# Kernel optimization log

Hardware: AMD Instinct MI355X
Metric: run time of the kernel (lower is better)

The kernel has to match this reference:

```python
import jax, jax.numpy as jnp
import numpy as np

N_NODES = 50000
N_EDGES = 200000
N_GRAPH = 1024
H = 128          # hidden_channels
POS = 48         # pos_offset
NF = 256         # num_filters in SchNetInteraction
L = 5            # n_layers
NFF = 512
MAX_ITEM = 300


def ssp(v):
    # shifted softplus used by SchNet
    return jax.nn.softplus(v) - jnp.log(2.0)


def setup_inputs() -> dict:
    key = jax.random.key(0)
    ks = iter(jax.random.split(key, 40))
    s = 0.05
    inp = {}
    inp['x'] = jax.random.randint(next(ks), (N_NODES,), 0, MAX_ITEM)
    inp['edge_index'] = jax.random.randint(next(ks), (2, N_EDGES), 0, N_NODES)
    inp['edge_attr'] = jax.random.normal(next(ks), (N_EDGES, 4), jnp.float32)
    inp['batch'] = jnp.sort(jax.random.randint(next(ks), (N_NODES,), 0, N_GRAPH))
    inp['pos'] = jax.random.normal(next(ks), (N_NODES, 3), jnp.float32)
    # embedding / projection params
    vert = jax.random.normal(next(ks), (MAX_ITEM + 1, H - POS), jnp.float32) * s
    inp['vert_emb'] = vert.at[MAX_ITEM].set(0.0)  # padding_idx
    inp['pos_w'] = jax.random.normal(next(ks), (POS, 3), jnp.float32) * s
    inp['edge_w'] = jax.random.normal(next(ks), (H, 4), jnp.float32) * s
    # per-layer SchNetInteraction params (stacked over L)
    inp['filt_w1'] = jax.random.normal(next(ks), (L, NF, H), jnp.float32) * s
    inp['filt_b1'] = jnp.zeros((L, NF), jnp.float32)
    inp['filt_w2'] = jax.random.normal(next(ks), (L, NF, NF), jnp.float32) * s
    inp['filt_b2'] = jnp.zeros((L, NF), jnp.float32)
    inp['lin1_w'] = jax.random.normal(next(ks), (L, NF, H), jnp.float32) * s
    inp['lin2_w'] = jax.random.normal(next(ks), (L, H, NF), jnp.float32) * s
    inp['lin2_b'] = jnp.zeros((L, H), jnp.float32)
    inp['lin3_w'] = jax.random.normal(next(ks), (L, H, H), jnp.float32) * s
    inp['lin3_b'] = jnp.zeros((L, H), jnp.float32)
    # per-layer edge MLP: Linear(edge_ch + in_ch -> in_ch) + Tanh
    inp['em_w'] = jax.random.normal(next(ks), (L, H, 2 * H), jnp.float32) * s
    inp['em_b'] = jnp.zeros((L, H), jnp.float32)
    # head
    inp['head_w1'] = jax.random.normal(next(ks), (NFF, H), jnp.float32) * s
    inp['head_b1'] = jnp.zeros((NFF,), jnp.float32)
    inp['head_w2'] = jax.random.normal(next(ks), (1, NFF), jnp.float32) * s
    inp['head_b2'] = jnp.zeros((1,), jnp.float32)
    return inp


def _forward(x, edge_index, edge_attr, batch, pos, vert_emb, pos_w, edge_w,
             filt_w1, filt_b1, filt_w2, filt_b2, lin1_w, lin2_w, lin2_b,
             lin3_w, lin3_b, em_w, em_b, head_w1, head_b1, head_w2, head_b2):
    n = x.shape[0]
    src, dst = edge_index[0], edge_index[1]
    h = jnp.concatenate([vert_emb[x], pos @ pos_w.T], axis=-1)  # [N, H]
    ea = edge_attr @ edge_w.T                                    # [E, H]
    for i in range(L):
        # SchNetInteraction / CFConv: per-edge filter MLP, gather, scatter-sum
        W = ssp(ea @ filt_w1[i].T + filt_b1[i]) @ filt_w2[i].T + filt_b2[i]  # [E, NF]
        hj = (h @ lin1_w[i].T)[src]                                          # [E, NF]
        agg = jax.ops.segment_sum(hj * W, dst, num_segments=n)               # [N, NF]
        out = ssp(agg @ lin2_w[i].T + lin2_b[i]) @ lin3_w[i].T + lin3_b[i]   # [N, H]
        h = jax.nn.relu(out) + h  # relu + residual skip
        # edge MLP update (always active in ResGraphModule)
        ea = jnp.tanh(jnp.concatenate([ea, h[src] + h[dst]], axis=-1) @ em_w[i].T + em_b[i]) + ea
    # global mean pool over graphs
    ssum = jax.ops.segment_sum(h, batch, num_segments=N_GRAPH)               # [G, H]
    cnt = jax.ops.segment_sum(jnp.ones((n,), h.dtype), batch, num_segments=N_GRAPH)
    g = ssum / jnp.maximum(cnt, 1.0)[:, None]
    # head: Linear -> GELU (exact, as torch default) -> Dropout(eval) -> Linear
    y = jax.nn.gelu(g @ head_w1.T + head_b1, approximate=False) @ head_w2.T + head_b2
    return y  # [G, 1]


def reference(x, edge_index, edge_attr, batch, pos, vert_emb, pos_w, edge_w,
              filt_w1, filt_b1, filt_w2, filt_b2, lin1_w, lin2_w, lin2_b,
              lin3_w, lin3_b, em_w, em_b, head_w1, head_b1, head_w2, head_b2):
    return _forward(x, edge_index, edge_attr, batch, pos, vert_emb, pos_w, edge_w,
                    filt_w1, filt_b1, filt_w2, filt_b2, lin1_w, lin2_w, lin2_b,
                    lin3_w, lin3_b, em_w, em_b, head_w1, head_b1, head_w2, head_b2)
```

## Files before the change

### kernel.cpp

```cpp
#include <hip/hip_runtime.h>
#include <hip/hip_bf16.h>
#include <math.h>

#define N_NODES 50000
#define N_EDGES 200000
#define N_GRAPH 1024
#define HC      128
#define NFC     256
#define NLAYER  5
#define NFFC    512

typedef short bf16x8 __attribute__((ext_vector_type(8)));
typedef float f4v    __attribute__((ext_vector_type(4)));

__device__ __forceinline__ float ssp_f(float x) {
  float e = __expf(-fabsf(x));
  return fmaxf(x, 0.0f) + __logf(1.0f + e) - 0.69314718055994530942f;
}
__device__ __forceinline__ float tanh_f(float x) {
  float e = __expf(2.0f * fabsf(x));
  float t = 1.0f - 2.0f * __builtin_amdgcn_rcpf(e + 1.0f);
  return copysignf(t, x);
}
__device__ __forceinline__ unsigned short f2bf(float x) {
  union { float f; unsigned u; } v; v.f = x;
  unsigned r = v.u + 0x7fff + ((v.u >> 16) & 1);
  return (unsigned short)(r >> 16);
}
__device__ __forceinline__ float bf2f(unsigned short b) {
  union { unsigned u; float f; } v; v.u = (unsigned)b << 16; return v.f;
}

__device__ __forceinline__ int swzA(int row, int col) {
  return (row << 7) + (((col >> 3) ^ (row & 7)) << 3) + (col & 7);
}
__device__ __forceinline__ int swzT(int row, int col) {
  return (row << 8) + (((col >> 3) ^ (row & 7)) << 3) + (col & 7);
}

__global__ void zero_kernel(float4* __restrict__ p, int n4) {
  int i = blockIdx.x * blockDim.x + threadIdx.x;
  if (i < n4) p[i] = make_float4(0.f, 0.f, 0.f, 0.f);
}
__global__ void zeroi_kernel(int* __restrict__ p, int n) {
  int i = blockIdx.x * blockDim.x + threadIdx.x;
  if (i < n) p[i] = 0;
}

__global__ void hist_kernel(const int* __restrict__ ei, int* __restrict__ deg) {
  int e = blockIdx.x * blockDim.x + threadIdx.x;
  if (e < N_EDGES) atomicAdd(&deg[ei[N_EDGES + e]], 1);
}
__global__ void scan1_kernel(const int* __restrict__ deg, int* __restrict__ excl,
                             int* __restrict__ bsum, int n) {
  __shared__ int buf[256];
  const int tid = threadIdx.x;
  const int i = blockIdx.x * 256 + tid;
  int v = (i < n) ? deg[i] : 0;
  buf[tid] = v;
  __syncthreads();
  for (int s = 1; s < 256; s <<= 1) {
    int t = (tid >= s) ? buf[tid - s] : 0;
    __syncthreads();
    buf[tid] += t;
    __syncthreads();
  }
  if (i < n) excl[i] = buf[tid] - v;
  if (tid == 255) bsum[blockIdx.x] = buf[255];
}
__global__ void scan2_kernel(int* __restrict__ bsum, int nb) {
  __shared__ int buf[256];
  const int tid = threadIdx.x;
  int v = (tid < nb) ? bsum[tid] : 0;
  buf[tid] = v;
  __syncthreads();
  for (int s = 1; s < 256; s <<= 1) {
    int t = (tid >= s) ? buf[tid - s] : 0;
    __syncthreads();
    buf[tid] += t;
    __syncthreads();
  }
  if (tid < nb) bsum[tid] = buf[tid] - v;
}
__global__ void scan3_kernel(int* __restrict__ excl, const int* __restrict__ bsum, int n) {
  int i = blockIdx.x * 256 + threadIdx.x;
  if (i < n) excl[i] += bsum[blockIdx.x];
}
__global__ void perm_kernel(const int* __restrict__ ei, int* __restrict__ cursor,
                            int* __restrict__ perm) {
  int e = blockIdx.x * blockDim.x + threadIdx.x;
  if (e < N_EDGES) {
    int d = ei[N_EDGES + e];
    int p = atomicAdd(&cursor[d], 1);
    perm[p] = e;
  }
}
__global__ void eperm_kernel(const int* __restrict__ ei, const int* __restrict__ perm,
                             int* __restrict__ eiPs, int* __restrict__ eiPd,
                             int* __restrict__ ipos) {
  int p = blockIdx.x * blockDim.x + threadIdx.x;
  if (p < N_EDGES) {
    int e = perm[p];
    eiPs[p] = ei[e];
    eiPd[p] = ei[N_EDGES + e];
    ipos[e] = p;
  }
}

__global__ void wconv_kernel(const float* __restrict__ w,
                             unsigned short* __restrict__ hi, int n) {
  int i = blockIdx.x * blockDim.x + threadIdx.x;
  if (i < n) hi[i] = f2bf(w[i]);
}

__global__ void embed_kernel(const int* __restrict__ x, const float* __restrict__ pos,
                             const float* __restrict__ vert, const float* __restrict__ posw,
                             unsigned short* __restrict__ h) {
  int n = blockIdx.x;
  int c = threadIdx.x;
  float v;
  if (c < 80) {
    v = vert[(size_t)x[n] * 80 + c];
  } else {
    int j = c - 80;
    v = pos[n*3+0]*posw[j*3+0] + pos[n*3+1]*posw[j*3+1] + pos[n*3+2]*posw[j*3+2];
  }
  h[(size_t)n*HC + c] = f2bf(v);
}

__global__ void edgeproj_kernel(const float* __restrict__ eattr, const float* __restrict__ ew,
                                unsigned short* __restrict__ eaP,
                                const int* __restrict__ ipos) {
  int idx = blockIdx.x * blockDim.x + threadIdx.x;
  if (idx >= N_EDGES * HC) return;
  int e = idx >> 7, c = idx & 127;
  const float* a = eattr + (size_t)e*4;
  const float* w = ew + (size_t)c*4;
  eaP[(size_t)ipos[e]*HC + c] = f2bf(a[0]*w[0] + a[1]*w[1] + a[2]*w[2] + a[3]*w[3]);
}

__global__ __launch_bounds__(256, 4) void emlite_kernel(
    unsigned short* eaP,
    const unsigned short* __restrict__ Bh,
    const float* __restrict__ bias,
    const int* __restrict__ eiPs, const int* __restrict__ eiPd,
    const unsigned short* __restrict__ hfeat)
{
  __shared__ unsigned short ldsA[64 * 128];
  __shared__ unsigned short ldsH[64 * 128];

  const int tid  = threadIdx.x;
  const int m0   = blockIdx.x * 64;
  const int lane = tid & 63, wave = tid >> 6;
  const int quad = lane >> 4, l16 = lane & 15;
  const int r = tid >> 2, cb = (tid & 3) * 32;

  const int e = m0 + r;
  const int s = eiPs[e], d = eiPd[e];

  {
    const unsigned short* ap = eaP + (size_t)e * HC + cb;
#pragma unroll
    for (int q = 0; q < 4; q++)
      *(bf16x8*)&ldsA[swzA(r, cb + q*8)] = *(const bf16x8*)(ap + q*8);
    const unsigned short* p1 = hfeat + (size_t)s * HC + cb;
    const unsigned short* p2 = hfeat + (size_t)d * HC + cb;
    unsigned short x1[32], x2[32], th[32];
#pragma unroll
    for (int q = 0; q < 4; q++) {
      *(bf16x8*)&x1[q*8] = *(const bf16x8*)(p1 + q*8);
      *(bf16x8*)&x2[q*8] = *(const bf16x8*)(p2 + q*8);
    }
#pragma unroll
    for (int j = 0; j < 32; j++) th[j] = f2bf(bf2f(x1[j]) + bf2f(x2[j]));
#pragma unroll
    for (int q = 0; q < 4; q++)
      *(bf16x8*)&ldsH[swzA(r, cb + q*8)] = *(bf16x8*)&th[q*8];
  }

  const f4v zf = {0.f, 0.f, 0.f, 0.f};
  f4v acc[4][2];
#pragma unroll
  for (int mt = 0; mt < 4; mt++) { acc[mt][0] = zf; acc[mt][1] = zf; }

  __syncthreads();

#pragma unroll
  for (int nt = 0; nt < 2; nt++) {
    const size_t brow = (size_t)(wave*32 + nt*16 + l16);
#pragma unroll
    for (int kk = 0; kk < 128; kk += 32) {
      bf16x8 b = *(const bf16x8*)&Bh[brow * 2*HC + kk + quad*8];
#pragma unroll
      for (int mt = 0; mt < 4; mt++) {
        bf16x8 a = *(const bf16x8*)&ldsA[swzA(mt*16 + l16, kk + quad*8)];
        acc[mt][nt] = __builtin_amdgcn_mfma_f32_16x16x32_bf16(a, b, acc[mt][nt], 0, 0, 0);
      }
    }
#pragma unroll
    for (int kk = 0; kk < 128; kk += 32) {
      bf16x8 b = *(const bf16x8*)&Bh[brow * 2*HC + HC + kk + quad*8];
#pragma unroll
      for (int mt = 0; mt < 4; mt++) {
        bf16x8 a = *(const bf16x8*)&ldsH[swzA(mt*16 + l16, kk + quad*8)];
        acc[mt][nt] = __builtin_amdgcn_mfma_f32_16x16x32_bf16(a, b, acc[mt][nt], 0, 0, 0);
      }
    }
  }

#pragma unroll
  for (int nt = 0; nt < 2; nt++) {
    const int col = wave*32 + nt*16 + l16;
    const float bz = bias[col];
#pragma unroll
    for (int mt = 0; mt < 4; mt++) {
      const int rowb = mt*16 + quad*4;
#pragma unroll
      for (int rr = 0; rr < 4; rr++) {
        const size_t idx = (size_t)(m0 + rowb + rr) * HC + col;
        eaP[idx] = f2bf(tanh_f(acc[mt][nt][rr] + bz) + bf2f(ldsA[swzA(rowb + rr, col)]));
      }
    }
  }
}

__global__ __launch_bounds__(256, 2) void nodeup_kernel(
    float* __restrict__ agg,
    const unsigned short* __restrict__ L2h,
    const float* __restrict__ b2,
    const unsigned short* __restrict__ L3h,
    const float* __restrict__ b3,
    unsigned short* h)
{
  __shared__ unsigned short ldsS[128 * 256];

  const int tid  = threadIdx.x;
  const int m0   = blockIdx.x * 128;
  const int lane = tid & 63, wave = tid >> 6;
  const int quad = lane >> 4, l16 = lane & 15;
  const int wm = (wave >> 1) * 64, wn = (wave & 1) * 64;
  const int r  = tid >> 1;
  const int ch = (tid & 1) * 128;

  const bool mok = (m0 + r) < N_NODES;

  if (mok) {
    const float* ap = agg + (size_t)(m0 + r) * NFC + ch;
#pragma unroll
    for (int g = 0; g < 16; g++) {
      float4 v0 = *(const float4*)(ap + g*8);
      float4 v1 = *(const float4*)(ap + g*8 + 4);
      unsigned short th[8];
      th[0] = f2bf(v0.x); th[1] = f2bf(v0.y); th[2] = f2bf(v0.z); th[3] = f2bf(v0.w);
      th[4] = f2bf(v1.x); th[5] = f2bf(v1.y); th[6] = f2bf(v1.z); th[7] = f2bf(v1.w);
      *(bf16x8*)&ldsS[swzT(r, ch + g*8)] = *(bf16x8*)th;
    }
    float4* zp = (float4*)(agg + (size_t)(m0 + r) * NFC + ch);
    const float4 z4 = make_float4(0.f, 0.f, 0.f, 0.f);
#pragma unroll
    for (int g = 0; g < 32; g++) zp[g] = z4;
  } else {
    const bf16x8 zb = {0, 0, 0, 0, 0, 0, 0, 0};
#pragma unroll
    for (int g = 0; g < 16; g++) *(bf16x8*)&ldsS[swzT(r, ch + g*8)] = zb;
  }

  const f4v zf = {0.f, 0.f, 0.f, 0.f};
  f4v acc[4][4];
#pragma unroll
  for (int i = 0; i < 4; i++)
#pragma unroll
    for (int j = 0; j < 4; j++) acc[i][j] = zf;

  __syncthreads();

  for (int kk = 0; kk < NFC; kk += 32) {
    bf16x8 b[4];
#pragma unroll
    for (int nt = 0; nt < 4; nt++) {
      const size_t brow = (size_t)(wn + nt*16 + l16);
      b[nt] = *(const bf16x8*)&L2h[brow * NFC + kk + quad*8];
    }
    bf16x8 a[4];
#pragma unroll
    for (int t = 0; t < 4; t++)
      a[t] = *(const bf16x8*)&ldsS[swzT(wm + t*16 + l16, kk + quad*8)];
#pragma unroll
    for (int mt = 0; mt < 4; mt++)
#pragma unroll
      for (int nt = 0; nt < 4; nt++)
        acc[mt][nt] = __builtin_amdgcn_mfma_f32_16x16x32_bf16(a[mt], b[nt], acc[mt][nt], 0, 0, 0);
  }
  __syncthreads();

#pragma unroll
  for (int nt = 0; nt < 4; nt++) {
    const int col = wn + nt*16 + l16;
    const float bz = b2[col];
#pragma unroll
    for (int mt = 0; mt < 4; mt++) {
      const int rowb = wm + mt*16 + quad*4;
#pragma unroll
      for (int rr = 0; rr < 4; rr++)
        ldsS[swzT(rowb+rr, col)] = f2bf(ssp_f(acc[mt][nt][rr] + bz));
    }
  }
  __syncthreads();

  f4v acc2[4][4];
#pragma unroll
  for (int i = 0; i < 4; i++)
#pragma unroll
    for (int j = 0; j < 4; j++) acc2[i][j] = zf;

  for (int kk = 0; kk < HC; kk += 32) {
    bf16x8 b[4];
#pragma unroll
    for (int nt = 0; nt < 4; nt++) {
      const size_t brow = (size_t)(wn + nt*16 + l16);
      b[nt] = *(const bf16x8*)&L3h[brow * HC + kk + quad*8];
    }
    bf16x8 a[4];
#pragma unroll
    for (int t = 0; t < 4; t++)
      a[t] = *(const bf16x8*)&ldsS[swzT(wm + t*16 + l16, kk + quad*8)];
#pragma unroll
    for (int mt = 0; mt < 4; mt++)
#pragma unroll
      for (int nt = 0; nt < 4; nt++)
        acc2[mt][nt] = __builtin_amdgcn_mfma_f32_16x16x32_bf16(a[mt], b[nt], acc2[mt][nt], 0, 0, 0);
  }

#pragma unroll
  for (int nt = 0; nt < 4; nt++) {
    const int ncol = wn + nt*16 + l16;
    const float bz = b3[ncol];
#pragma unroll
    for (int mt = 0; mt < 4; mt++) {
      const int mb = wm + mt*16 + quad*4;
#pragma unroll
      for (int rr = 0; rr < 4; rr++) {
        const int m = m0 + mb + rr;
        if (m < N_NODES) {
          const size_t idx = (size_t)m * HC + ncol;
          h[idx] = f2bf(fmaxf(acc2[mt][nt][rr] + bz, 0.f) + bf2f(h[idx]));
        }
      }
    }
  }
}

__device__ __forceinline__ int sigma_row(int r) {
  return ((r >> 2) & 3) * 16 + (r >> 4) * 4 + (r & 3);
}
__global__ __launch_bounds__(256, 3) void ffs_kernel(
    const unsigned short* __restrict__ eaP,
    const unsigned short* __restrict__ l1h,
    const unsigned short* __restrict__ fw1h,
    const float* __restrict__ fb1,
    const unsigned short* __restrict__ fw2h,
    const float* __restrict__ fb2,
    const int* __restrict__ eiPs, const int* __restrict__ eiPd,
    const unsigned short* __restrict__ hfeat, float* __restrict__ agg)
{
  __shared__ unsigned short ldsA[64 * 128];
  __shared__ unsigned short ldsT[64 * 256];
  __shared__ int sD[64];

  const int tid  = threadIdx.x;
  const int m0   = blockIdx.x * 64;
  const int lane = tid & 63, wave = tid >> 6;
  const int quad = lane >> 4, l16 = lane & 15;
  const int r = tid >> 2, cb = (tid & 3) * 32;
  const int sp = m0 + sigma_row(r);

  const int s = eiPs[sp];
  bf16x8 hreg[4];
  {
    const unsigned short* hp = hfeat + (size_t)s * HC + cb;
#pragma unroll
    for (int q = 0; q < 4; q++) hreg[q] = *(const bf16x8*)(hp + q*8);
  }
  if (tid < 64) sD[tid] = eiPd[m0 + sigma_row(tid)];

  {
    const unsigned short* ap = eaP + (size_t)sp * HC + cb;
#pragma unroll
    for (int q = 0; q < 4; q++)
      *(bf16x8*)&ldsA[swzA(r, cb + q*8)] = *(const bf16x8*)(ap + q*8);
  }

  const f4v zf = {0.f, 0.f, 0.f, 0.f};
  __syncthreads();

  for (int p = 0; p < 4; p++) {
    f4v tacc[4];
#pragma unroll
    for (int mt = 0; mt < 4; mt++) tacc[mt] = zf;
    const size_t b1row = (size_t)(p*64 + wave*16 + l16);
#pragma unroll
    for (int kk = 0; kk < 128; kk += 32) {
      bf16x8 b = *(const bf16x8*)&fw1h[b1row * HC + kk + quad*8];
#pragma unroll
      for (int mt = 0; mt < 4; mt++) {
        bf16x8 a = *(const bf16x8*)&ldsA[swzA(mt*16 + l16, kk + quad*8)];
        tacc[mt] = __builtin_amdgcn_mfma_f32_16x16x32_bf16(a, b, tacc[mt], 0, 0, 0);
      }
    }
    const int col = p*64 + wave*16 + l16;
    const float bz = fb1[col];
#pragma unroll
    for (int mt = 0; mt < 4; mt++) {
      const int rowb = mt*16 + quad*4;
#pragma unroll
      for (int rr = 0; rr < 4; rr++)
        ldsT[swzT(rowb+rr, col)] = f2bf(ssp_f(tacc[mt][rr] + bz));
    }
  }
  __syncthreads();

#pragma unroll
  for (int q = 0; q < 4; q++)
    *(bf16x8*)&ldsA[swzA(r, cb + q*8)] = hreg[q];

  f4v wacc[4][4];
#pragma unroll
  for (int mt = 0; mt < 4; mt++)
#pragma unroll
    for (int nt = 0; nt < 4; nt++) wacc[mt][nt] = zf;

  __builtin_amdgcn_s_setprio(1);
  for (int p = 0; p < 4; p++) {
#pragma unroll
    for (int kc = 0; kc < 2; kc++) {
      bf16x8 a_[4];
#pragma unroll
      for (int mt = 0; mt < 4; mt++)
        a_[mt] = *(const bf16x8*)&ldsT[swzT(mt*16 + l16, p*64 + kc*32 + quad*8)];
#pragma unroll
      for (int nt = 0; nt < 4; nt++) {
        const size_t brow = (size_t)(wave*64 + nt*16 + l16);
        bf16x8 b = *(const bf16x8*)&fw2h[brow * NFC + p*64 + kc*32 + quad*8];
#pragma unroll
        for (int mt = 0; mt < 4; mt++)
          wacc[mt][nt] = __builtin_amdgcn_mfma_f32_16x16x32_bf16(a_[mt], b, wacc[mt][nt], 0, 0, 0);
      }
    }
  }
  __builtin_amdgcn_s_setprio(0);
  __syncthreads();

  f4v hacc[4][4];
#pragma unroll
  for (int mt = 0; mt < 4; mt++)
#pragma unroll
    for (int nt = 0; nt < 4; nt++) hacc[mt][nt] = zf;

#pragma unroll
  for (int kk = 0; kk < 128; kk += 32) {
    bf16x8 a_[4];
#pragma unroll
    for (int mt = 0; mt < 4; mt++)
      a_[mt] = *(const bf16x8*)&ldsA[swzA(mt*16 + l16, kk + quad*8)];
#pragma unroll
    for (int nt = 0; nt < 4; nt++) {
      const size_t brow = (size_t)(wave*64 + nt*16 + l16);
      bf16x8 b = *(const bf16x8*)&l1h[brow * HC + kk + quad*8];
#pragma unroll
      for (int mt = 0; mt < 4; mt++)
        hacc[mt][nt] = __builtin_amdgcn_mfma_f32_16x16x32_bf16(a_[mt], b, hacc[mt][nt], 0, 0, 0);
    }
  }

#pragma unroll
  for (int nt = 0; nt < 4; nt++) {
    const int col = wave*64 + nt*16 + l16;
    const float bz = fb2[col];
    float accum = 0.f;
    int prev = -1;
    bool firstrun = true;
#pragma unroll
    for (int mt = 0; mt < 4; mt++) {
#pragma unroll
      for (int rr = 0; rr < 4; rr++) {
        const int prow = mt*16 + quad*4 + rr;
        const int d = sD[prow];
        const float v = (wacc[mt][nt][rr] + bz) * hacc[mt][nt][rr];
        if (d != prev) {
          if (prev >= 0) {
            if (firstrun) atomicAdd(&agg[(size_t)prev * NFC + col], accum);
            else          agg[(size_t)prev * NFC + col] = accum;
            firstrun = false;
          }
          accum = v; prev = d;
        } else {
          accum += v;
        }
      }
    }
    atomicAdd(&agg[(size_t)prev * NFC + col], accum);
  }
}

__global__ __launch_bounds__(256) void poolhead_kernel(
    const int* __restrict__ batch, const unsigned short* __restrict__ h,
    const float* __restrict__ w1, const float* __restrict__ b1,
    const float* __restrict__ w2, const float* __restrict__ b2,
    float* __restrict__ y)
{
  __shared__ float gs[HC];
  __shared__ float red[256];
  const int g = blockIdx.x;
  const int tid = threadIdx.x;

  int lo = 0, hi = N_NODES;
  while (lo < hi) { int m = (lo + hi) >> 1; if (batch[m] < g) lo = m + 1; else hi = m; }
  int lo2 = lo, hi2 = N_NODES;
  while (lo2 < hi2) { int m = (lo2 + hi2) >> 1; if (batch[m] < g + 1) lo2 = m + 1; else hi2 = m; }
  const int cnt = lo2 - lo;

  if (tid < HC) {
    float s = 0.f;
    for (int i = lo; i < lo2; i++) s += bf2f(h[(size_t)i * HC + tid]);
    gs[tid] = s / (float)max(cnt, 1);
  }
  __syncthreads();

  float partial = 0.f;
  for (int f = tid; f < NFFC; f += 256) {
    float acc = b1[f];
    const float* wr = w1 + (size_t)f * HC;
#pragma unroll 8
    for (int k = 0; k < HC; k++) acc = fmaf(gs[k], wr[k], acc);
    float t = 0.5f * acc * (1.0f + erff(acc * 0.70710678118654752440f));
    partial = fmaf(t, w2[f], partial);
  }
  red[tid] = partial;
  __syncthreads();
  for (int s = 128; s > 0; s >>= 1) {
    if (tid < s) red[tid] += red[tid + s];
    __syncthreads();
  }
  if (tid == 0) y[g] = red[0] + b2[0];
}

extern "C" void kernel_launch(void* const* d_in, const int* in_sizes, int n_in,
                              void* d_out, int out_size, void* d_ws, size_t ws_size,
                              hipStream_t stream) {
  const int*   x     = (const int*)  d_in[0];
  const int*   ei    = (const int*)  d_in[1];
  const float* eattr = (const float*)d_in[2];
  const int*   batch = (const int*)  d_in[3];
  const float* pos   = (const float*)d_in[4];
  const float* vert  = (const float*)d_in[5];
  const float* posw  = (const float*)d_in[6];
  const float* edgew = (const float*)d_in[7];
  const float* fw1   = (const float*)d_in[8];
  const float* fb1   = (const float*)d_in[9];
  const float* fw2   = (const float*)d_in[10];
  const float* fb2   = (const float*)d_in[11];
  const float* l1w   = (const float*)d_in[12];
  const float* l2w   = (const float*)d_in[13];
  const float* l2b   = (const float*)d_in[14];
  const float* l3w   = (const float*)d_in[15];
  const float* l3b   = (const float*)d_in[16];
  const float* emw   = (const float*)d_in[17];
  const float* emb   = (const float*)d_in[18];
  const float* hw1   = (const float*)d_in[19];
  const float* hb1   = (const float*)d_in[20];
  const float* hw2   = (const float*)d_in[21];
  const float* hb2   = (const float*)d_in[22];
  float* out = (float*)d_out;

  char* ws = (char*)d_ws;
  size_t off = 0;
  auto alloc = [&](size_t bytes) { char* p = ws + off; off += (bytes + 511) & ~(size_t)511; return p; };
  unsigned short* eaP = (unsigned short*)alloc((size_t)N_EDGES*HC*2);
  unsigned short* h   = (unsigned short*)alloc((size_t)N_NODES*HC*2);
  float* agg  = (float*)alloc((size_t)N_NODES*NFC*4);
  int* deg    = (int*)alloc((size_t)(N_NODES+1)*4);
  int* cursor = (int*)alloc((size_t)(N_NODES+1)*4);
  int* bsum   = (int*)alloc((size_t)256*4);
  int* perm   = (int*)alloc((size_t)N_EDGES*4);
  int* eiPs   = (int*)alloc((size_t)N_EDGES*4);
  int* eiPd   = (int*)alloc((size_t)N_EDGES*4);
  int* ipos   = (int*)alloc((size_t)N_EDGES*4);
  const int n_fw1 = NLAYER*NFC*HC, n_fw2 = NLAYER*NFC*NFC, n_l1 = NLAYER*NFC*HC;
  const int n_l2 = NLAYER*HC*NFC, n_l3 = NLAYER*HC*HC, n_em = NLAYER*HC*2*HC;
  unsigned short* fw1h = (unsigned short*)alloc((size_t)n_fw1*2);
  unsigned short* fw2h = (unsigned short*)alloc((size_t)n_fw2*2);
  unsigned short* l1h  = (unsigned short*)alloc((size_t)n_l1*2);
  unsigned short* l2h  = (unsigned short*)alloc((size_t)n_l2*2);
  unsigned short* l3h  = (unsigned short*)alloc((size_t)n_l3*2);
  unsigned short* emh  = (unsigned short*)alloc((size_t)n_em*2);

  const int NSCAN = N_NODES + 1;
  const int NB    = (NSCAN + 255) / 256;

  zeroi_kernel<<<(NSCAN+255)/256, 256, 0, stream>>>(deg, NSCAN);
  hist_kernel<<<(N_EDGES+255)/256, 256, 0, stream>>>(ei, deg);
  scan1_kernel<<<NB, 256, 0, stream>>>(deg, cursor, bsum, NSCAN);
  scan2_kernel<<<1, 256, 0, stream>>>(bsum, NB);
  scan3_kernel<<<NB, 256, 0, stream>>>(cursor, bsum, NSCAN);
  perm_kernel<<<(N_EDGES+255)/256, 256, 0, stream>>>(ei, cursor, perm);
  eperm_kernel<<<(N_EDGES+255)/256, 256, 0, stream>>>(ei, perm, eiPs, eiPd, ipos);

  wconv_kernel<<<(n_fw1+255)/256, 256, 0, stream>>>(fw1, fw1h, n_fw1);
  wconv_kernel<<<(n_fw2+255)/256, 256, 0, stream>>>(fw2, fw2h, n_fw2);
  wconv_kernel<<<(n_l1 +255)/256, 256, 0, stream>>>(l1w, l1h, n_l1);
  wconv_kernel<<<(n_l2 +255)/256, 256, 0, stream>>>(l2w, l2h, n_l2);
  wconv_kernel<<<(n_l3 +255)/256, 256, 0, stream>>>(l3w, l3h, n_l3);
  wconv_kernel<<<(n_em +255)/256, 256, 0, stream>>>(emw, emh, n_em);

  const int GN   = (N_NODES + 127) / 128;
  const int GE64 = N_EDGES / 64;

  embed_kernel<<<N_NODES, 128, 0, stream>>>(x, pos, vert, posw, h);
  edgeproj_kernel<<<(N_EDGES*HC + 255)/256, 256, 0, stream>>>(eattr, edgew, eaP, ipos);
  zero_kernel<<<((N_NODES*NFC/4) + 255)/256, 256, 0, stream>>>(
      (float4*)agg, N_NODES*NFC/4);

  for (int i = 0; i < NLAYER; ++i) {
    ffs_kernel<<<GE64, 256, 0, stream>>>(
        eaP, l1h + (size_t)i*NFC*HC,
        fw1h + (size_t)i*NFC*HC, fb1 + (size_t)i*NFC,
        fw2h + (size_t)i*NFC*NFC, fb2 + (size_t)i*NFC,
        eiPs, eiPd, h, agg);
    nodeup_kernel<<<GN, 256, 0, stream>>>(
        agg, l2h + (size_t)i*HC*NFC, l2b + (size_t)i*HC,
        l3h + (size_t)i*HC*HC, l3b + (size_t)i*HC, h);
    if (i < NLAYER - 1) {
      emlite_kernel<<<GE64, 256, 0, stream>>>(
          eaP, emh + (size_t)i*HC*2*HC, emb + (size_t)i*HC,
          eiPs, eiPd, h);
    }
  }

  poolhead_kernel<<<N_GRAPH, 256, 0, stream>>>(batch, h, hw1, hb1, hw2, hb2, out);
}
```

Baseline: 1.485 ms.

## Prefetch weight fragments across MFMA loops and shrink nodeup tile for occupancy

Adds one-step-ahead register prefetch of global B-operand fragments in the edge-MLP, filter (ffs) and node-update kernels, so weight loads overlap MFMA work instead of stalling. The ffs kernel splits its W/H accumulators into two column halves, which cuts live registers. The node-update kernel moves to 64-row tiles with 4 blocks per CU and half the shared memory, doubling the grid. The risk is lower per-block weight reuse and the extra syncs and loop overhead of the half-split.

```diff
diff --git a/kernel.cpp b/kernel.cpp
--- a/kernel.cpp
+++ b/kernel.cpp
@@ -183,28 +183,25 @@
 #pragma unroll
   for (int mt = 0; mt < 4; mt++) { acc[mt][0] = zf; acc[mt][1] = zf; }
 
-  __syncthreads();
-
-#pragma unroll
-  for (int nt = 0; nt < 2; nt++) {
-    const size_t brow = (size_t)(wave*32 + nt*16 + l16);
-#pragma unroll
-    for (int kk = 0; kk < 128; kk += 32) {
-      bf16x8 b = *(const bf16x8*)&Bh[brow * 2*HC + kk + quad*8];
-#pragma unroll
-      for (int mt = 0; mt < 4; mt++) {
-        bf16x8 a = *(const bf16x8*)&ldsA[swzA(mt*16 + l16, kk + quad*8)];
-        acc[mt][nt] = __builtin_amdgcn_mfma_f32_16x16x32_bf16(a, b, acc[mt][nt], 0, 0, 0);
-      }
-    }
-#pragma unroll
-    for (int kk = 0; kk < 128; kk += 32) {
-      bf16x8 b = *(const bf16x8*)&Bh[brow * 2*HC + HC + kk + quad*8];
-#pragma unroll
-      for (int mt = 0; mt < 4; mt++) {
-        bf16x8 a = *(const bf16x8*)&ldsH[swzA(mt*16 + l16, kk + quad*8)];
-        acc[mt][nt] = __builtin_amdgcn_mfma_f32_16x16x32_bf16(a, b, acc[mt][nt], 0, 0, 0);
-      }
+  bf16x8 bn = *(const bf16x8*)&Bh[(size_t)(wave*32 + l16) * 2*HC + quad*8];
+
+  __syncthreads();
+
+#pragma unroll
+  for (int g = 0; g < 16; g++) {
+    const int nt = g >> 3, hf = (g >> 2) & 1, ki = g & 3;
+    bf16x8 bc = bn;
+    if (g < 15) {
+      const int g1 = g + 1;
+      const int nt1 = g1 >> 3, hf1 = (g1 >> 2) & 1, ki1 = g1 & 3;
+      bn = *(const bf16x8*)&Bh[(size_t)(wave*32 + nt1*16 + l16) * 2*HC
+                               + hf1*HC + ki1*32 + quad*8];
+    }
+    const unsigned short* src = hf ? ldsH : ldsA;
+#pragma unroll
+    for (int mt = 0; mt < 4; mt++) {
+      bf16x8 a = *(const bf16x8*)&src[swzA(mt*16 + l16, ki*32 + quad*8)];
+      acc[mt][nt] = __builtin_amdgcn_mfma_f32_16x16x32_bf16(a, bc, acc[mt][nt], 0, 0, 0);
     }
   }
 
@@ -224,7 +221,7 @@
   }
 }
 
-__global__ __launch_bounds__(256, 2) void nodeup_kernel(
+__global__ __launch_bounds__(256, 4) void nodeup_kernel(
     float* __restrict__ agg,
     const unsigned short* __restrict__ L2h,
     const float* __restrict__ b2,
@@ -232,112 +229,121 @@
     const float* __restrict__ b3,
     unsigned short* h)
 {
-  __shared__ unsigned short ldsS[128 * 256];
+  __shared__ unsigned short ldsS[64 * 256];
 
   const int tid  = threadIdx.x;
-  const int m0   = blockIdx.x * 128;
+  const int m0   = blockIdx.x * 64;
   const int lane = tid & 63, wave = tid >> 6;
   const int quad = lane >> 4, l16 = lane & 15;
-  const int wm = (wave >> 1) * 64, wn = (wave & 1) * 64;
-  const int r  = tid >> 1;
-  const int ch = (tid & 1) * 128;
+  const int wn = wave * 32;
+  const int r  = tid >> 2;
+  const int cb2 = (tid & 3) * 64;
 
   const bool mok = (m0 + r) < N_NODES;
 
   if (mok) {
-    const float* ap = agg + (size_t)(m0 + r) * NFC + ch;
-#pragma unroll
-    for (int g = 0; g < 16; g++) {
+    const float* ap = agg + (size_t)(m0 + r) * NFC + cb2;
+#pragma unroll
+    for (int g = 0; g < 8; g++) {
       float4 v0 = *(const float4*)(ap + g*8);
       float4 v1 = *(const float4*)(ap + g*8 + 4);
       unsigned short th[8];
       th[0] = f2bf(v0.x); th[1] = f2bf(v0.y); th[2] = f2bf(v0.z); th[3] = f2bf(v0.w);
       th[4] = f2bf(v1.x); th[5] = f2bf(v1.y); th[6] = f2bf(v1.z); th[7] = f2bf(v1.w);
-      *(bf16x8*)&ldsS[swzT(r, ch + g*8)] = *(bf16x8*)th;
-    }
-    float4* zp = (float4*)(agg + (size_t)(m0 + r) * NFC + ch);
+      *(bf16x8*)&ldsS[swzT(r, cb2 + g*8)] = *(bf16x8*)th;
+    }
+    float4* zp = (float4*)(agg + (size_t)(m0 + r) * NFC + cb2);
     const float4 z4 = make_float4(0.f, 0.f, 0.f, 0.f);
 #pragma unroll
-    for (int g = 0; g < 32; g++) zp[g] = z4;
+    for (int g = 0; g < 16; g++) zp[g] = z4;
   } else {
     const bf16x8 zb = {0, 0, 0, 0, 0, 0, 0, 0};
 #pragma unroll
-    for (int g = 0; g < 16; g++) *(bf16x8*)&ldsS[swzT(r, ch + g*8)] = zb;
+    for (int g = 0; g < 8; g++) *(bf16x8*)&ldsS[swzT(r, cb2 + g*8)] = zb;
   }
 
   const f4v zf = {0.f, 0.f, 0.f, 0.f};
-  f4v acc[4][4];
-#pragma unroll
-  for (int i = 0; i < 4; i++)
-#pragma unroll
-    for (int j = 0; j < 4; j++) acc[i][j] = zf;
-
-  __syncthreads();
-
-  for (int kk = 0; kk < NFC; kk += 32) {
-    bf16x8 b[4];
-#pragma unroll
-    for (int nt = 0; nt < 4; nt++) {
-      const size_t brow = (size_t)(wn + nt*16 + l16);
-      b[nt] = *(const bf16x8*)&L2h[brow * NFC + kk + quad*8];
+  f4v acc[4][2];
+#pragma unroll
+  for (int i = 0; i < 4; i++) { acc[i][0] = zf; acc[i][1] = zf; }
+
+  bf16x8 bn[2];
+#pragma unroll
+  for (int nt = 0; nt < 2; nt++)
+    bn[nt] = *(const bf16x8*)&L2h[(size_t)(wn + nt*16 + l16) * NFC + quad*8];
+
+  __syncthreads();
+
+  for (int kki = 0; kki < 8; kki++) {
+    bf16x8 bc[2] = {bn[0], bn[1]};
+    if (kki < 7) {
+#pragma unroll
+      for (int nt = 0; nt < 2; nt++)
+        bn[nt] = *(const bf16x8*)&L2h[(size_t)(wn + nt*16 + l16) * NFC
+                                      + (kki+1)*32 + quad*8];
     }
     bf16x8 a[4];
 #pragma unroll
     for (int t = 0; t < 4; t++)
-      a[t] = *(const bf16x8*)&ldsS[swzT(wm + t*16 + l16, kk + quad*8)];
+      a[t] = *(const bf16x8*)&ldsS[swzT(t*16 + l16, kki*32 + quad*8)];
 #pragma unroll
     for (int mt = 0; mt < 4; mt++)
 #pragma unroll
-      for (int nt = 0; nt < 4; nt++)
-        acc[mt][nt] = __builtin_amdgcn_mfma_f32_16x16x32_bf16(a[mt], b[nt], acc[mt][nt], 0, 0, 0);
-  }
-  __syncthreads();
-
-#pragma unroll
-  for (int nt = 0; nt < 4; nt++) {
+      for (int nt = 0; nt < 2; nt++)
+        acc[mt][nt] = __builtin_amdgcn_mfma_f32_16x16x32_bf16(a[mt], bc[nt], acc[mt][nt], 0, 0, 0);
+  }
+  __syncthreads();
+
+#pragma unroll
+  for (int nt = 0; nt < 2; nt++) {
     const int col = wn + nt*16 + l16;
     const float bz = b2[col];
 #pragma unroll
     for (int mt = 0; mt < 4; mt++) {
-      const int rowb = wm + mt*16 + quad*4;
+      const int rowb = mt*16 + quad*4;
 #pragma unroll
       for (int rr = 0; rr < 4; rr++)
-        ldsS[swzT(rowb+rr, col)] = f2bf(ssp_f(acc[mt][nt][rr] + bz));
-    }
-  }
-  __syncthreads();
-
-  f4v acc2[4][4];
-#pragma unroll
-  for (int i = 0; i < 4; i++)
-#pragma unroll
-    for (int j = 0; j < 4; j++) acc2[i][j] = zf;
-
-  for (int kk = 0; kk < HC; kk += 32) {
-    bf16x8 b[4];
-#pragma unroll
-    for (int nt = 0; nt < 4; nt++) {
-      const size_t brow = (size_t)(wn + nt*16 + l16);
-      b[nt] = *(const bf16x8*)&L3h[brow * HC + kk + quad*8];
+        ldsS[swzA(rowb+rr, col)] = f2bf(ssp_f(acc[mt][nt][rr] + bz));
+    }
+  }
+
+  bf16x8 b3n[2];
+#pragma unroll
+  for (int nt = 0; nt < 2; nt++)
+    b3n[nt] = *(const bf16x8*)&L3h[(size_t)(wn + nt*16 + l16) * HC + quad*8];
+
+  __syncthreads();
+
+  f4v acc2[4][2];
+#pragma unroll
+  for (int i = 0; i < 4; i++) { acc2[i][0] = zf; acc2[i][1] = zf; }
+
+  for (int kki = 0; kki < 4; kki++) {
+    bf16x8 bc[2] = {b3n[0], b3n[1]};
+    if (kki < 3) {
+#pragma unroll
+      for (int nt = 0; nt < 2; nt++)
+        b3n[nt] = *(const bf16x8*)&L3h[(size_t)(wn + nt*16 + l16) * HC
+                                       + (kki+1)*32 + quad*8];
     }
     bf16x8 a[4];
 #pragma unroll
     for (int t = 0; t < 4; t++)
-      a[t] = *(const bf16x8*)&ldsS[swzT(wm + t*16 + l16, kk + quad*8)];
+      a[t] = *(const bf16x8*)&ldsS[swzA(t*16 + l16, kki*32 + quad*8)];
 #pragma unroll
     for (int mt = 0; mt < 4; mt++)
 #pragma unroll
-      for (int nt = 0; nt < 4; nt++)
-        acc2[mt][nt] = __builtin_amdgcn_mfma_f32_16x16x32_bf16(a[mt], b[nt], acc2[mt][nt], 0, 0, 0);
-  }
-
-#pragma unroll
-  for (int nt = 0; nt < 4; nt++) {
+      for (int nt = 0; nt < 2; nt++)
+        acc2[mt][nt] = __builtin_amdgcn_mfma_f32_16x16x32_bf16(a[mt], bc[nt], acc2[mt][nt], 0, 0, 0);
+  }
+
+#pragma unroll
+  for (int nt = 0; nt < 2; nt++) {
     const int ncol = wn + nt*16 + l16;
     const float bz = b3[ncol];
 #pragma unroll
     for (int mt = 0; mt < 4; mt++) {
-      const int mb = wm + mt*16 + quad*4;
+      const int mb = mt*16 + quad*4;
 #pragma unroll
       for (int rr = 0; rr < 4; rr++) {
         const int m = m0 + mb + rr;
@@ -391,23 +397,31 @@
   }
 
   const f4v zf = {0.f, 0.f, 0.f, 0.f};
+  const int bcol = wave*16 + l16;
+
+  bf16x8 b1n = *(const bf16x8*)&fw1h[(size_t)bcol * HC + quad*8];
+
   __syncthreads();
 
   for (int p = 0; p < 4; p++) {
     f4v tacc[4];
 #pragma unroll
     for (int mt = 0; mt < 4; mt++) tacc[mt] = zf;
-    const size_t b1row = (size_t)(p*64 + wave*16 + l16);
-#pragma unroll
-    for (int kk = 0; kk < 128; kk += 32) {
-      bf16x8 b = *(const bf16x8*)&fw1h[b1row * HC + kk + quad*8];
+#pragma unroll
+    for (int ki = 0; ki < 4; ki++) {
+      bf16x8 bc = b1n;
+      {
+        const int np = (ki < 3) ? p : ((p < 3) ? p + 1 : 3);
+        const int nk = (ki < 3) ? (ki + 1) * 32 : 0;
+        b1n = *(const bf16x8*)&fw1h[(size_t)(np*64 + bcol) * HC + nk + quad*8];
+      }
 #pragma unroll
       for (int mt = 0; mt < 4; mt++) {
-        bf16x8 a = *(const bf16x8*)&ldsA[swzA(mt*16 + l16, kk + quad*8)];
-        tacc[mt] = __builtin_amdgcn_mfma_f32_16x16x32_bf16(a, b, tacc[mt], 0, 0, 0);
+        bf16x8 a = *(const bf16x8*)&ldsA[swzA(mt*16 + l16, ki*32 + quad*8)];
+        tacc[mt] = __builtin_amdgcn_mfma_f32_16x16x32_bf16(a, bc, tacc[mt], 0, 0, 0);
       }
     }
-    const int col = p*64 + wave*16 + l16;
+    const int col = p*64 + bcol;
     const float bz = fb1[col];
 #pragma unroll
     for (int mt = 0; mt < 4; mt++) {
@@ -417,88 +431,113 @@
         ldsT[swzT(rowb+rr, col)] = f2bf(ssp_f(tacc[mt][rr] + bz));
     }
   }
+
+  bf16x8 b2n[2];
+#pragma unroll
+  for (int nt = 0; nt < 2; nt++)
+    b2n[nt] = *(const bf16x8*)&fw2h[(size_t)(wave*64 + nt*16 + l16) * NFC + quad*8];
+  bf16x8 b3n[2];
+#pragma unroll
+  for (int nt = 0; nt < 2; nt++)
+    b3n[nt] = *(const bf16x8*)&l1h[(size_t)(wave*64 + nt*16 + l16) * HC + quad*8];
+
   __syncthreads();
 
 #pragma unroll
   for (int q = 0; q < 4; q++)
     *(bf16x8*)&ldsA[swzA(r, cb + q*8)] = hreg[q];
 
-  f4v wacc[4][4];
-#pragma unroll
-  for (int mt = 0; mt < 4; mt++)
-#pragma unroll
-    for (int nt = 0; nt < 4; nt++) wacc[mt][nt] = zf;
-
-  __builtin_amdgcn_s_setprio(1);
-  for (int p = 0; p < 4; p++) {
-#pragma unroll
-    for (int kc = 0; kc < 2; kc++) {
+  __syncthreads();
+
+  for (int hf = 0; hf < 2; hf++) {
+    f4v wacc[4][2], hacc[4][2];
+#pragma unroll
+    for (int mt = 0; mt < 4; mt++) {
+      wacc[mt][0] = zf; wacc[mt][1] = zf;
+      hacc[mt][0] = zf; hacc[mt][1] = zf;
+    }
+
+    __builtin_amdgcn_s_setprio(1);
+    for (int g = 0; g < 8; g++) {
+      bf16x8 bc[2] = {b2n[0], b2n[1]};
+      if (g < 7) {
+        const int g1 = g + 1;
+        const int off = (g1 >> 1) * 64 + (g1 & 1) * 32;
+#pragma unroll
+        for (int nt = 0; nt < 2; nt++)
+          b2n[nt] = *(const bf16x8*)&fw2h[(size_t)(wave*64 + (hf*2+nt)*16 + l16) * NFC
+                                          + off + quad*8];
+      } else if (hf == 0) {
+#pragma unroll
+        for (int nt = 0; nt < 2; nt++)
+          b2n[nt] = *(const bf16x8*)&fw2h[(size_t)(wave*64 + (2+nt)*16 + l16) * NFC
+                                          + quad*8];
+      }
+      const int off0 = (g >> 1) * 64 + (g & 1) * 32;
       bf16x8 a_[4];
 #pragma unroll
       for (int mt = 0; mt < 4; mt++)
-        a_[mt] = *(const bf16x8*)&ldsT[swzT(mt*16 + l16, p*64 + kc*32 + quad*8)];
-#pragma unroll
-      for (int nt = 0; nt < 4; nt++) {
-        const size_t brow = (size_t)(wave*64 + nt*16 + l16);
-        bf16x8 b = *(const bf16x8*)&fw2h[brow * NFC + p*64 + kc*32 + quad*8];
+        a_[mt] = *(const bf16x8*)&ldsT[swzT(mt*16 + l16, off0 + quad*8)];
+#pragma unroll
+      for (int nt = 0; nt < 2; nt++)
 #pragma unroll
         for (int mt = 0; mt < 4; mt++)
-          wacc[mt][nt] = __builtin_amdgcn_mfma_f32_16x16x32_bf16(a_[mt], b, wacc[mt][nt], 0, 0, 0);
+          wacc[mt][nt] = __builtin_amdgcn_mfma_f32_16x16x32_bf16(a_[mt], bc[nt], wacc[mt][nt], 0, 0, 0);
+    }
+
+    for (int ki = 0; ki < 4; ki++) {
+      bf16x8 bc[2] = {b3n[0], b3n[1]};
+      if (ki < 3) {
+#pragma unroll
+        for (int nt = 0; nt < 2; nt++)
+          b3n[nt] = *(const bf16x8*)&l1h[(size_t)(wave*64 + (hf*2+nt)*16 + l16) * HC
+                                         + (ki+1)*32 + quad*8];
+      } else if (hf == 0) {
+#pragma unroll
+        for (int nt = 0; nt < 2; nt++)
+          b3n[nt] = *(const bf16x8*)&l1h[(size_t)(wave*64 + (2+nt)*16 + l16) * HC
+                                         + quad*8];
       }
-    }
-  }
-  __builtin_amdgcn_s_setprio(0);
-  __syncthreads();
-
-  f4v hacc[4][4];
-#pragma unroll
-  for (int mt = 0; mt < 4; mt++)
-#pragma unroll
-    for (int nt = 0; nt < 4; nt++) hacc[mt][nt] = zf;
-
-#pragma unroll
-  for (int kk = 0; kk < 128; kk += 32) {
-    bf16x8 a_[4];
-#pragma unroll
-    for (int mt = 0; mt < 4; mt++)
-      a_[mt] = *(const bf16x8*)&ldsA[swzA(mt*16 + l16, kk + quad*8)];
-#pragma unroll
-    for (int nt = 0; nt < 4; nt++) {
-      const size_t brow = (size_t)(wave*64 + nt*16 + l16);
-      bf16x8 b = *(const bf16x8*)&l1h[brow * HC + kk + quad*8];
+      bf16x8 a_[4];
 #pragma unroll
       for (int mt = 0; mt < 4; mt++)
-        hacc[mt][nt] = __builtin_amdgcn_mfma_f32_16x16x32_bf16(a_[mt], b, hacc[mt][nt], 0, 0, 0);
-    }
-  }
-
-#pragma unroll
-  for (int nt = 0; nt < 4; nt++) {
-    const int col = wave*64 + nt*16 + l16;
-    const float bz = fb2[col];
-    float accum = 0.f;
-    int prev = -1;
-    bool firstrun = true;
-#pragma unroll
-    for (int mt = 0; mt < 4; mt++) {
-#pragma unroll
-      for (int rr = 0; rr < 4; rr++) {
-        const int prow = mt*16 + quad*4 + rr;
-        const int d = sD[prow];
-        const float v = (wacc[mt][nt][rr] + bz) * hacc[mt][nt][rr];
-        if (d != prev) {
-          if (prev >= 0) {
-            if (firstrun) atomicAdd(&agg[(size_t)prev * NFC + col], accum);
-            else          agg[(size_t)prev * NFC + col] = accum;
-            firstrun = false;
+        a_[mt] = *(const bf16x8*)&ldsA[swzA(mt*16 + l16, ki*32 + quad*8)];
+#pragma unroll
+      for (int nt = 0; nt < 2; nt++)
+#pragma unroll
+        for (int mt = 0; mt < 4; mt++)
+          hacc[mt][nt] = __builtin_amdgcn_mfma_f32_16x16x32_bf16(a_[mt], bc[nt], hacc[mt][nt], 0, 0, 0);
+    }
+    __builtin_amdgcn_s_setprio(0);
+
+#pragma unroll
+    for (int nt = 0; nt < 2; nt++) {
+      const int col = wave*64 + (hf*2 + nt)*16 + l16;
+      const float bz = fb2[col];
+      float accum = 0.f;
+      int prev = -1;
+      bool firstrun = true;
+#pragma unroll
+      for (int mt = 0; mt < 4; mt++) {
+#pragma unroll
+        for (int rr = 0; rr < 4; rr++) {
+          const int prow = mt*16 + quad*4 + rr;
+          const int d = sD[prow];
+          const float v = (wacc[mt][nt][rr] + bz) * hacc[mt][nt][rr];
+          if (d != prev) {
+            if (prev >= 0) {
+              if (firstrun) atomicAdd(&agg[(size_t)prev * NFC + col], accum);
+              else          agg[(size_t)prev * NFC + col] = accum;
+              firstrun = false;
+            }
+            accum = v; prev = d;
+          } else {
+            accum += v;
           }
-          accum = v; prev = d;
-        } else {
-          accum += v;
         }
       }
-    }
-    atomicAdd(&agg[(size_t)prev * NFC + col], accum);
+      atomicAdd(&agg[(size_t)prev * NFC + col], accum);
+    }
   }
 }
 
@@ -612,7 +651,7 @@
   wconv_kernel<<<(n_l3 +255)/256, 256, 0, stream>>>(l3w, l3h, n_l3);
   wconv_kernel<<<(n_em +255)/256, 256, 0, stream>>>(emw, emh, n_em);
 
-  const int GN   = (N_NODES + 127) / 128;
+  const int GN   = (N_NODES + 63) / 64;
   const int GE64 = N_EDGES / 64;
 
   embed_kernel<<<N_NODES, 128, 0, stream>>>(x, pos, vert, posw, h);
```

Measured after the change: 2.521 ms. +69.8%, slower.
